# Kernel optimization log

Measured on AMD Instinct MI355X. Metric: run time of the kernel, lower is better.

Reference implementation:

```python
import jax, jax.numpy as jnp
import numpy as np

NUM_HEADS = 8
MODEL_DIM = 512
HIDDEN_DIM = 64  # model_dim // num_heads
BATCH = 4
SEQ = 1024


def setup_inputs() -> dict:
    key = jax.random.key(0)
    kx, kq, kk, kv, ko = jax.random.split(key, 5)
    # xavier_uniform bound for [model_dim, hidden_dim] fan pair
    bqkv = float(np.sqrt(6.0 / (MODEL_DIM + HIDDEN_DIM)))
    bo = float(np.sqrt(6.0 / (MODEL_DIM + MODEL_DIM)))
    return {
        "X": jax.random.normal(kx, (BATCH, SEQ, MODEL_DIM), dtype=jnp.float32),
        "mask": jnp.zeros((SEQ, SEQ), dtype=bool),  # unused by module
        "Wq": jax.random.uniform(kq, (NUM_HEADS, MODEL_DIM, HIDDEN_DIM), minval=-bqkv, maxval=bqkv, dtype=jnp.float32),
        "Wk": jax.random.uniform(kk, (NUM_HEADS, MODEL_DIM, HIDDEN_DIM), minval=-bqkv, maxval=bqkv, dtype=jnp.float32),
        "Wv": jax.random.uniform(kv, (NUM_HEADS, MODEL_DIM, HIDDEN_DIM), minval=-bqkv, maxval=bqkv, dtype=jnp.float32),
        "Wo": jax.random.uniform(ko, (MODEL_DIM, MODEL_DIM), minval=-bo, maxval=bo, dtype=jnp.float32),
    }


def reference(X, mask, Wq, Wk, Wv, Wo):
    # Per-head projections (replaces the replicated-tensor lin_proj with one einsum)
    q = jnp.einsum("bsm,hmd->hbsd", X, Wq)  # [h,b,s,d]
    k = jnp.einsum("bsm,hmd->hbsd", X, Wk)
    v = jnp.einsum("bsm,hmd->hbsd", X, Wv)
    # Katharopoulos feature map on q and k
    q = jax.nn.elu(q) + 1.0
    k = jax.nn.elu(k) + 1.0
    # Cumulative outer-product state S_t = sum_{i<=t} k_i v_i^T  -> [h,b,s,d,d]
    S = jnp.cumsum(k[..., :, None] * v[..., None, :], axis=2)
    V_bar = jnp.einsum("hbsd,hbsde->hbse", q, S)  # numerator
    Z = jnp.einsum("hbsd,hbsd->hbs", q, jnp.cumsum(k, axis=2))  # normalizer
    out_heads = V_bar / Z[..., None]  # [h,b,s,d]
    # combine_heads: permute to [b,s,h,d], flatten heads, project by Wo
    b, s = out_heads.shape[1], out_heads.shape[2]
    combined = jnp.transpose(out_heads, (1, 2, 0, 3)).reshape(b, s, -1)
    return jnp.einsum("bsm,mn->bsn", combined, Wo)
```

## Files before the change

### kernel.cpp

```cpp
#include <hip/hip_runtime.h>
#include <math.h>

namespace {
typedef unsigned short u16;
typedef __attribute__((ext_vector_type(8))) short bf16x8;
typedef __attribute__((ext_vector_type(4))) float f32x4;

constexpr int H  = 8;
constexpr int B  = 4;
constexpr int S  = 1024;
constexpr int M  = 512;
constexpr int D  = 64;
constexpr int BS = B * S;
constexpr int NC = 16;
constexpr int CH = 64;
constexpr int QSZ = H * B * S * D;
constexpr int NQKV = 3 * M;

__device__ __forceinline__ float elu1(float x) {
  return x > 0.f ? x + 1.f : __expf(x);
}

__device__ __forceinline__ u16 f2bf(float f) {
  unsigned u = __builtin_bit_cast(unsigned, f);
  u += 0x7fffu + ((u >> 16) & 1u);
  return (u16)(u >> 16);
}

__device__ __forceinline__ float bf2f(u16 v) {
  return __builtin_bit_cast(float, ((unsigned)v) << 16);
}

__device__ __forceinline__ void gload16(const u16* g, u16* l) {
  __builtin_amdgcn_global_load_lds(
      (const __attribute__((address_space(1))) unsigned int*)g,
      (__attribute__((address_space(3))) unsigned int*)l, 16, 0, 0);
}

__global__ __launch_bounds__(256) void convert_x(const float* __restrict__ X,
                                                 u16* __restrict__ Xb) {
  const int i = blockIdx.x * 256 + threadIdx.x;
  const float4 v = reinterpret_cast<const float4*>(X)[i];
  u16 o[4] = {f2bf(v.x), f2bf(v.y), f2bf(v.z), f2bf(v.w)};
  *reinterpret_cast<uint2*>(Xb + i * 4) = *reinterpret_cast<uint2*>(o);
}

__global__ __launch_bounds__(256) void build_wqkv(
    const float* __restrict__ Wq, const float* __restrict__ Wk,
    const float* __restrict__ Wv, u16* __restrict__ WCT) {
  __shared__ float t[64][65];
  const int p = blockIdx.y >> 3, h = blockIdx.y & 7;
  const float* W = ((p == 0) ? Wq : (p == 1) ? Wk : Wv) + h * (M * D);
  const int m0 = blockIdx.x * 64;
#pragma unroll
  for (int j = 0; j < 4; ++j) {
    const int i = j * 256 + threadIdx.x;
    const int mm = i >> 4, dd = (i & 15) * 4;
    const float4 v = *reinterpret_cast<const float4*>(W + (m0 + mm) * D + dd);
    t[mm][dd + 0] = v.x; t[mm][dd + 1] = v.y;
    t[mm][dd + 2] = v.z; t[mm][dd + 3] = v.w;
  }
  __syncthreads();
  const int dd = threadIdx.x >> 2, qr = (threadIdx.x & 3) * 16;
  u16* o = WCT + (p * M + h * D + dd) * M + m0 + qr;
#pragma unroll
  for (int i = 0; i < 16; ++i) o[i] = f2bf(t[qr + i][dd]);
}

__global__ __launch_bounds__(256) void build_wo(const float* __restrict__ Wo,
                                                u16* __restrict__ WoT) {
  __shared__ float t[64][65];
  const int m0 = blockIdx.x * 64, n0 = blockIdx.y * 64;
#pragma unroll
  for (int j = 0; j < 4; ++j) {
    const int i = j * 256 + threadIdx.x;
    const int mm = i >> 4, nn = (i & 15) * 4;
    const float4 v = *reinterpret_cast<const float4*>(Wo + (m0 + mm) * M + n0 + nn);
    t[mm][nn + 0] = v.x; t[mm][nn + 1] = v.y;
    t[mm][nn + 2] = v.z; t[mm][nn + 3] = v.w;
  }
  __syncthreads();
  const int nn = threadIdx.x >> 2, qr = (threadIdx.x & 3) * 16;
  u16* o = WoT + (n0 + nn) * M + m0 + qr;
#pragma unroll
  for (int i = 0; i < 16; ++i) o[i] = f2bf(t[qr + i][nn]);
}

__global__ __launch_bounds__(256) void gemm_qkv(const u16* __restrict__ A,
                                                const u16* __restrict__ BT,
                                                u16* __restrict__ qb,
                                                u16* __restrict__ kb,
                                                u16* __restrict__ kTb,
                                                u16* __restrict__ vTb) {
  __shared__ alignas(16) u16 As[128 * 32];
  __shared__ alignas(16) u16 Bs[128 * 32];
  const int tid = threadIdx.x;
  const int wave = tid >> 6, lane = tid & 63;
  const int r0 = blockIdx.x * 128, c0 = blockIdx.y * 128;
  const int wr = (wave >> 1) * 64, wc = (wave & 1) * 64;

  f32x4 acc[4][4] = {};
  const int lrow = tid >> 2;
  const int lk = (tid & 3) * 8;
  const u16* ga0 = A + (size_t)(r0 + lrow) * 512 + lk;
  const u16* ga1 = A + (size_t)(r0 + 64 + lrow) * 512 + lk;
  const u16* gb0 = BT + (size_t)(c0 + lrow) * 512 + lk;
  const u16* gb1 = BT + (size_t)(c0 + 64 + lrow) * 512 + lk;
  u16* lA0 = &As[wave * 512];
  u16* lA1 = &As[2048 + wave * 512];
  u16* lB0 = &Bs[wave * 512];
  u16* lB1 = &Bs[2048 + wave * 512];

  for (int kt = 0; kt < 16; ++kt) {
    __syncthreads();
    const int ko = kt * 32;
    gload16(ga0 + ko, lA0);
    gload16(ga1 + ko, lA1);
    gload16(gb0 + ko, lB0);
    gload16(gb1 + ko, lB1);
    __syncthreads();
    const bf16x8* As8 = reinterpret_cast<const bf16x8*>(As);
    const bf16x8* Bs8 = reinterpret_cast<const bf16x8*>(Bs);
    bf16x8 af[4], bff[4];
#pragma unroll
    for (int mf = 0; mf < 4; ++mf)
      af[mf] = As8[(wr + mf * 16 + (lane & 15)) * 4 + (lane >> 4)];
#pragma unroll
    for (int nf = 0; nf < 4; ++nf)
      bff[nf] = Bs8[(wc + nf * 16 + (lane & 15)) * 4 + (lane >> 4)];
#pragma unroll
    for (int mf = 0; mf < 4; ++mf)
#pragma unroll
      for (int nf = 0; nf < 4; ++nf)
        acc[mf][nf] = __builtin_amdgcn_mfma_f32_16x16x32_bf16(
            af[mf], bff[nf], acc[mf][nf], 0, 0, 0);
  }

#pragma unroll
  for (int nf = 0; nf < 4; ++nf) {
    const int col = c0 + wc + nf * 16 + (lane & 15);
    const int p = col >> 9, hh = (col >> 6) & 7, dd = col & 63;
#pragma unroll
    for (int mf = 0; mf < 4; ++mf) {
      const int rowb = r0 + wr + mf * 16 + (lane >> 4) * 4;
      const int b = rowb >> 10, s = rowb & 1023;
      const int hb = hh * B + b;
      u16 ov[4];
#pragma unroll
      for (int r = 0; r < 4; ++r) {
        float v = acc[mf][nf][r];
        if (p < 2) v = elu1(v);
        ov[r] = f2bf(v);
      }
      if (p == 0) {
#pragma unroll
        for (int r = 0; r < 4; ++r)
          qb[((size_t)(hb << 10) + s + r) * 64 + dd] = ov[r];
      } else if (p == 1) {
#pragma unroll
        for (int r = 0; r < 4; ++r)
          kb[((size_t)(hb << 10) + s + r) * 64 + dd] = ov[r];
        *reinterpret_cast<uint2*>(kTb + ((size_t)(hb * 64 + dd) << 10) + s) =
            *reinterpret_cast<uint2*>(ov);
      } else {
        *reinterpret_cast<uint2*>(vTb + ((size_t)(hb * 64 + dd) << 10) + s) =
            *reinterpret_cast<uint2*>(ov);
      }
    }
  }
}

__global__ __launch_bounds__(256) void gemm_out(const u16* __restrict__ A,
                                                const u16* __restrict__ BT,
                                                float* __restrict__ out) {
  __shared__ alignas(16) u16 As[128 * 32];
  __shared__ alignas(16) u16 Bs[128 * 32];
  const int tid = threadIdx.x;
  const int wave = tid >> 6, lane = tid & 63;
  const int r0 = blockIdx.x * 128, c0 = blockIdx.y * 128;
  const int wr = (wave >> 1) * 64, wc = (wave & 1) * 64;

  f32x4 acc[4][4] = {};
  const int lrow = tid >> 2;
  const int lk = (tid & 3) * 8;
  const u16* ga0 = A + (size_t)(r0 + lrow) * 512 + lk;
  const u16* ga1 = A + (size_t)(r0 + 64 + lrow) * 512 + lk;
  const u16* gb0 = BT + (size_t)(c0 + lrow) * 512 + lk;
  const u16* gb1 = BT + (size_t)(c0 + 64 + lrow) * 512 + lk;
  u16* lA0 = &As[wave * 512];
  u16* lA1 = &As[2048 + wave * 512];
  u16* lB0 = &Bs[wave * 512];
  u16* lB1 = &Bs[2048 + wave * 512];

  for (int kt = 0; kt < 16; ++kt) {
    __syncthreads();
    const int ko = kt * 32;
    gload16(ga0 + ko, lA0);
    gload16(ga1 + ko, lA1);
    gload16(gb0 + ko, lB0);
    gload16(gb1 + ko, lB1);
    __syncthreads();
    const bf16x8* As8 = reinterpret_cast<const bf16x8*>(As);
    const bf16x8* Bs8 = reinterpret_cast<const bf16x8*>(Bs);
    bf16x8 af[4], bff[4];
#pragma unroll
    for (int mf = 0; mf < 4; ++mf)
      af[mf] = As8[(wr + mf * 16 + (lane & 15)) * 4 + (lane >> 4)];
#pragma unroll
    for (int nf = 0; nf < 4; ++nf)
      bff[nf] = Bs8[(wc + nf * 16 + (lane & 15)) * 4 + (lane >> 4)];
#pragma unroll
    for (int mf = 0; mf < 4; ++mf)
#pragma unroll
      for (int nf = 0; nf < 4; ++nf)
        acc[mf][nf] = __builtin_amdgcn_mfma_f32_16x16x32_bf16(
            af[mf], bff[nf], acc[mf][nf], 0, 0, 0);
  }
#pragma unroll
  for (int nf = 0; nf < 4; ++nf) {
    const int col = c0 + wc + nf * 16 + (lane & 15);
#pragma unroll
    for (int mf = 0; mf < 4; ++mf)
#pragma unroll
      for (int r = 0; r < 4; ++r) {
        const int row = r0 + wr + mf * 16 + (lane >> 4) * 4 + r;
        out[(size_t)row * M + col] = acc[mf][nf][r];
      }
  }
}

__global__ __launch_bounds__(256) void chunkstate_mfma(
    const u16* __restrict__ kTb, const u16* __restrict__ vTb,
    float* __restrict__ G32, float* __restrict__ Ks) {
  const int tid = threadIdx.x, wave = tid >> 6, lane = tid & 63;
  const int bx = blockIdx.x, hb = bx >> 4, cc = bx & 15, s0 = cc * CH;
  const u16* vbase = vTb + ((size_t)hb * 64) * 1024 + s0;
  const u16* kbase = kTb + ((size_t)hb * 64) * 1024 + s0;

  bf16x8 av[2];
#pragma unroll
  for (int ks = 0; ks < 2; ++ks)
    av[ks] = *reinterpret_cast<const bf16x8*>(
        vbase + (size_t)(wave * 16 + (lane & 15)) * 1024 + ks * 32 + (lane >> 4) * 8);

  f32x4 acc[4] = {};
#pragma unroll
  for (int fd = 0; fd < 4; ++fd)
#pragma unroll
    for (int ks = 0; ks < 2; ++ks) {
      bf16x8 bk = *reinterpret_cast<const bf16x8*>(
          kbase + (size_t)(fd * 16 + (lane & 15)) * 1024 + ks * 32 + (lane >> 4) * 8);
      acc[fd] = __builtin_amdgcn_mfma_f32_16x16x32_bf16(av[ks], bk, acc[fd], 0, 0, 0);
    }

  float* Gp = G32 + (size_t)bx * 4096;
#pragma unroll
  for (int fd = 0; fd < 4; ++fd)
#pragma unroll
    for (int r = 0; r < 4; ++r) {
      const int e = wave * 16 + (lane >> 4) * 4 + r;
      const int d = fd * 16 + (lane & 15);
      Gp[e * 64 + d] = acc[fd][r];
    }

  const int d = tid >> 2, tq = tid & 3;
  const u16* kp = kbase + (size_t)d * 1024 + tq * 16;
  float ks = 0.f;
#pragma unroll
  for (int j = 0; j < 16; ++j) ks += bf2f(kp[j]);
  ks += __shfl_xor(ks, 1);
  ks += __shfl_xor(ks, 2);
  if (tq == 0) Ks[bx * 64 + d] = ks;
}

__global__ __launch_bounds__(256) void prefix_kernel(
    const float* __restrict__ G32, u16* __restrict__ GTb,
    float* __restrict__ Ks) {
  const int hb = blockIdx.x, eg = blockIdx.y;
  const int tid = threadIdx.x;
  const int e = eg * 4 + (tid >> 6), d = tid & 63;
  const size_t base = ((size_t)(hb * 16) * 64 + e) * 64 + d;
  float acc = 0.f;
#pragma unroll
  for (int c = 0; c < 16; ++c) {
    const float v = G32[base + (size_t)c * 4096];
    GTb[base + (size_t)c * 4096] = f2bf(acc);
    acc += v;
  }
  if (eg == 0 && tid < 64) {
    float ka = 0.f;
#pragma unroll
    for (int c = 0; c < 16; ++c) {
      const int idx = (hb * 16 + c) * 64 + tid;
      const float v = Ks[idx];
      Ks[idx] = ka;
      ka += v;
    }
  }
}

__global__ __launch_bounds__(256) void chunkout_mfma(
    const u16* __restrict__ qb, const u16* __restrict__ kb,
    const u16* __restrict__ vTb, const u16* __restrict__ GTb,
    const float* __restrict__ Kc, u16* __restrict__ att) {
  __shared__ alignas(16) u16 Qs[4096], Kls[4096], Vs[4096], Gs[4096], Astg[4096];
  const int tid = threadIdx.x, wave = tid >> 6, lane = tid & 63;
  const int bx = blockIdx.x, hb = bx >> 4, cc = bx & 15, s0 = cc * CH;
  const int h = hb >> 2, b = hb & 3;

  {
    const u16* qg = qb + ((size_t)(hb << 10) + s0) * 64;
    const u16* kg = kb + ((size_t)(hb << 10) + s0) * 64;
    const u16* gg = GTb + (size_t)bx * 4096;
#pragma unroll
    for (int j = 0; j < 2; ++j) {
      const int off = j * 2048 + wave * 512;
      gload16(qg + off + lane * 8, Qs + off);
      gload16(kg + off + lane * 8, Kls + off);
      gload16(gg + off + lane * 8, Gs + off);
    }
    const u16* vg = vTb + ((size_t)hb * 64) * 1024 + s0;
#pragma unroll
    for (int j = 0; j < 2; ++j) {
      const int e0 = j * 32 + wave * 8;
      gload16(vg + (size_t)(e0 + (lane >> 3)) * 1024 + (lane & 7) * 8,
              Vs + e0 * 64);
    }
  }
  __syncthreads();

  const bf16x8* Qs8 = reinterpret_cast<const bf16x8*>(Qs);
  const bf16x8* Ks8 = reinterpret_cast<const bf16x8*>(Kls);
  const bf16x8* Vs8 = reinterpret_cast<const bf16x8*>(Vs);
  const bf16x8* Gs8 = reinterpret_cast<const bf16x8*>(Gs);
  const bf16x8* As8 = reinterpret_cast<const bf16x8*>(Astg);

  const int i0 = wave * 16;
  const int l15 = lane & 15, lk = lane >> 4;

  bf16x8 aq[2];
#pragma unroll
  for (int ks = 0; ks < 2; ++ks)
    aq[ks] = Qs8[(i0 + l15) * 8 + ks * 4 + lk];

  f32x4 a[4] = {};
#pragma unroll
  for (int fj = 0; fj < 4; ++fj)
#pragma unroll
    for (int ks = 0; ks < 2; ++ks) {
      bf16x8 bk = Ks8[(fj * 16 + l15) * 8 + ks * 4 + lk];
      a[fj] = __builtin_amdgcn_mfma_f32_16x16x32_bf16(aq[ks], bk, a[fj], 0, 0, 0);
    }

  const float4 kc4 = *reinterpret_cast<const float4*>(Kc + bx * 64 + l15 * 4);
  float z[4];
  const int rbase = lk * 4;
#pragma unroll
  for (int r = 0; r < 4; ++r) {
    const int il = rbase + r;
    float sum = 0.f;
#pragma unroll
    for (int fj = 0; fj < 4; ++fj) {
      const int j = fj * 16 + l15;
      if (j > i0 + il) a[fj][r] = 0.f;
      sum += a[fj][r];
    }
    const uint2 qrow = *reinterpret_cast<const uint2*>(Qs + (i0 + il) * 64 + l15 * 4);
    const u16* qr16 = reinterpret_cast<const u16*>(&qrow);
    sum += bf2f(qr16[0]) * kc4.x + bf2f(qr16[1]) * kc4.y +
           bf2f(qr16[2]) * kc4.z + bf2f(qr16[3]) * kc4.w;
    z[r] = sum;
  }
#pragma unroll
  for (int off = 1; off <= 8; off <<= 1)
#pragma unroll
    for (int r = 0; r < 4; ++r) z[r] += __shfl_xor(z[r], off);

#pragma unroll
  for (int fj = 0; fj < 4; ++fj)
#pragma unroll
    for (int r = 0; r < 4; ++r)
      Astg[(i0 + rbase + r) * 64 + fj * 16 + l15] = f2bf(a[fj][r]);
  __syncthreads();

  f32x4 o[4] = {};
#pragma unroll
  for (int fe = 0; fe < 4; ++fe) {
#pragma unroll
    for (int ks = 0; ks < 2; ++ks) {
      bf16x8 bg = Gs8[(fe * 16 + l15) * 8 + ks * 4 + lk];
      o[fe] = __builtin_amdgcn_mfma_f32_16x16x32_bf16(aq[ks], bg, o[fe], 0, 0, 0);
    }
#pragma unroll
    for (int ks = 0; ks < 2; ++ks) {
      bf16x8 aa = As8[(i0 + l15) * 8 + ks * 4 + lk];
      bf16x8 bv = Vs8[(fe * 16 + l15) * 8 + ks * 4 + lk];
      o[fe] = __builtin_amdgcn_mfma_f32_16x16x32_bf16(aa, bv, o[fe], 0, 0, 0);
    }
  }

  float rz[4];
#pragma unroll
  for (int r = 0; r < 4; ++r) rz[r] = 1.f / z[r];
#pragma unroll
  for (int fe = 0; fe < 4; ++fe)
#pragma unroll
    for (int r = 0; r < 4; ++r) {
      const int srow = s0 + i0 + rbase + r;
      att[((size_t)(b << 10) + srow) * 512 + h * 64 + fe * 16 + l15] =
          f2bf(o[fe][r] * rz[r]);
    }
}

}

extern "C" void kernel_launch(void* const* d_in, const int* in_sizes, int n_in,
                              void* d_out, int out_size, void* d_ws,
                              size_t ws_size, hipStream_t stream) {
  const float* X  = (const float*)d_in[0];
  const float* Wq = (const float*)d_in[2];
  const float* Wk = (const float*)d_in[3];
  const float* Wv = (const float*)d_in[4];
  const float* Wo = (const float*)d_in[5];
  float* out = (float*)d_out;

  u16* Xb  = (u16*)d_ws;
  u16* att = Xb;
  u16* WCT = Xb + QSZ;
  u16* WoT = WCT + NQKV * M;
  u16* qb  = WoT + M * M;
  u16* kb  = qb + QSZ;
  u16* kTb = kb + QSZ;
  u16* vTb = kTb + QSZ;
  u16* GTb = vTb + QSZ;
  float* G32 = (float*)(GTb + QSZ);
  float* Ks  = G32 + QSZ;

  convert_x<<<dim3(QSZ / 1024), 256, 0, stream>>>(X, Xb);
  build_wqkv<<<dim3(8, 24), 256, 0, stream>>>(Wq, Wk, Wv, WCT);
  build_wo<<<dim3(8, 8), 256, 0, stream>>>(Wo, WoT);
  gemm_qkv<<<dim3(BS / 128, NQKV / 128), 256, 0, stream>>>(Xb, WCT, qb, kb,
                                                           kTb, vTb);
  chunkstate_mfma<<<dim3(H * B * NC), 256, 0, stream>>>(kTb, vTb, G32, Ks);
  prefix_kernel<<<dim3(H * B, 16), 256, 0, stream>>>(G32, GTb, Ks);
  chunkout_mfma<<<dim3(H * B * NC), 256, 0, stream>>>(qb, kb, vTb, GTb, Ks,
                                                      att);
  gemm_out<<<dim3(BS / 128, M / 128), 256, 0, stream>>>(att, WoT, out);
}
```

Baseline: 60.58 us.

## Merge prep kernels, fuse chunk state with prefix scan, retile both GEMMs

Folds the three input-conversion kernels into one launch that dispatches on block index. Merges the chunk-state and prefix kernels into a single per-head-batch kernel that walks the 16 chunks in order and keeps the running state in registers, which removes the fp32 intermediate buffer and one launch. Both GEMMs move to smaller output tiles (64x128 and 64x64) with a K step of 64, giving more blocks to fill the GPU. The fused state kernel launches only 32 blocks and runs its chunks one after another, which may underuse the device.

```diff
diff --git a/kernel.cpp b/kernel.cpp
--- a/kernel.cpp
+++ b/kernel.cpp
@@ -37,53 +37,54 @@
       (__attribute__((address_space(3))) unsigned int*)l, 16, 0, 0);
 }
 
-__global__ __launch_bounds__(256) void convert_x(const float* __restrict__ X,
-                                                 u16* __restrict__ Xb) {
-  const int i = blockIdx.x * 256 + threadIdx.x;
-  const float4 v = reinterpret_cast<const float4*>(X)[i];
-  u16 o[4] = {f2bf(v.x), f2bf(v.y), f2bf(v.z), f2bf(v.w)};
-  *reinterpret_cast<uint2*>(Xb + i * 4) = *reinterpret_cast<uint2*>(o);
-}
-
-__global__ __launch_bounds__(256) void build_wqkv(
-    const float* __restrict__ Wq, const float* __restrict__ Wk,
-    const float* __restrict__ Wv, u16* __restrict__ WCT) {
+__global__ __launch_bounds__(256) void prep(
+    const float* __restrict__ X, const float* __restrict__ Wq,
+    const float* __restrict__ Wk, const float* __restrict__ Wv,
+    const float* __restrict__ Wo, u16* __restrict__ Xb,
+    u16* __restrict__ WCT, u16* __restrict__ WoT) {
   __shared__ float t[64][65];
-  const int p = blockIdx.y >> 3, h = blockIdx.y & 7;
-  const float* W = ((p == 0) ? Wq : (p == 1) ? Wk : Wv) + h * (M * D);
-  const int m0 = blockIdx.x * 64;
-#pragma unroll
-  for (int j = 0; j < 4; ++j) {
-    const int i = j * 256 + threadIdx.x;
-    const int mm = i >> 4, dd = (i & 15) * 4;
-    const float4 v = *reinterpret_cast<const float4*>(W + (m0 + mm) * D + dd);
-    t[mm][dd + 0] = v.x; t[mm][dd + 1] = v.y;
-    t[mm][dd + 2] = v.z; t[mm][dd + 3] = v.w;
-  }
-  __syncthreads();
-  const int dd = threadIdx.x >> 2, qr = (threadIdx.x & 3) * 16;
-  u16* o = WCT + (p * M + h * D + dd) * M + m0 + qr;
-#pragma unroll
-  for (int i = 0; i < 16; ++i) o[i] = f2bf(t[qr + i][dd]);
-}
-
-__global__ __launch_bounds__(256) void build_wo(const float* __restrict__ Wo,
-                                                u16* __restrict__ WoT) {
-  __shared__ float t[64][65];
-  const int m0 = blockIdx.x * 64, n0 = blockIdx.y * 64;
-#pragma unroll
-  for (int j = 0; j < 4; ++j) {
-    const int i = j * 256 + threadIdx.x;
-    const int mm = i >> 4, nn = (i & 15) * 4;
-    const float4 v = *reinterpret_cast<const float4*>(Wo + (m0 + mm) * M + n0 + nn);
-    t[mm][nn + 0] = v.x; t[mm][nn + 1] = v.y;
-    t[mm][nn + 2] = v.z; t[mm][nn + 3] = v.w;
-  }
-  __syncthreads();
-  const int nn = threadIdx.x >> 2, qr = (threadIdx.x & 3) * 16;
-  u16* o = WoT + (n0 + nn) * M + m0 + qr;
-#pragma unroll
-  for (int i = 0; i < 16; ++i) o[i] = f2bf(t[qr + i][nn]);
+  const int bid = blockIdx.x;
+  if (bid < 2048) {
+    const int i = bid * 256 + threadIdx.x;
+    const float4 v = reinterpret_cast<const float4*>(X)[i];
+    u16 o[4] = {f2bf(v.x), f2bf(v.y), f2bf(v.z), f2bf(v.w)};
+    *reinterpret_cast<uint2*>(Xb + i * 4) = *reinterpret_cast<uint2*>(o);
+  } else if (bid < 2240) {
+    const int bb = bid - 2048;
+    const int mt = bb & 7, ph = bb >> 3;
+    const int p = ph >> 3, h = ph & 7;
+    const float* W = ((p == 0) ? Wq : (p == 1) ? Wk : Wv) + h * (M * D);
+    const int m0 = mt * 64;
+#pragma unroll
+    for (int j = 0; j < 4; ++j) {
+      const int i = j * 256 + threadIdx.x;
+      const int mm = i >> 4, dd = (i & 15) * 4;
+      const float4 v = *reinterpret_cast<const float4*>(W + (m0 + mm) * D + dd);
+      t[mm][dd + 0] = v.x; t[mm][dd + 1] = v.y;
+      t[mm][dd + 2] = v.z; t[mm][dd + 3] = v.w;
+    }
+    __syncthreads();
+    const int dd = threadIdx.x >> 2, qr = (threadIdx.x & 3) * 16;
+    u16* o = WCT + (p * M + h * D + dd) * M + m0 + qr;
+#pragma unroll
+    for (int i = 0; i < 16; ++i) o[i] = f2bf(t[qr + i][dd]);
+  } else {
+    const int bb = bid - 2240;
+    const int m0 = (bb & 7) * 64, n0 = (bb >> 3) * 64;
+#pragma unroll
+    for (int j = 0; j < 4; ++j) {
+      const int i = j * 256 + threadIdx.x;
+      const int mm = i >> 4, nn = (i & 15) * 4;
+      const float4 v = *reinterpret_cast<const float4*>(Wo + (m0 + mm) * M + n0 + nn);
+      t[mm][nn + 0] = v.x; t[mm][nn + 1] = v.y;
+      t[mm][nn + 2] = v.z; t[mm][nn + 3] = v.w;
+    }
+    __syncthreads();
+    const int nn = threadIdx.x >> 2, qr = (threadIdx.x & 3) * 16;
+    u16* o = WoT + (n0 + nn) * M + m0 + qr;
+#pragma unroll
+    for (int i = 0; i < 16; ++i) o[i] = f2bf(t[qr + i][nn]);
+  }
 }
 
 __global__ __launch_bounds__(256) void gemm_qkv(const u16* __restrict__ A,
@@ -92,59 +93,60 @@
                                                 u16* __restrict__ kb,
                                                 u16* __restrict__ kTb,
                                                 u16* __restrict__ vTb) {
-  __shared__ alignas(16) u16 As[128 * 32];
-  __shared__ alignas(16) u16 Bs[128 * 32];
-  const int tid = threadIdx.x;
-  const int wave = tid >> 6, lane = tid & 63;
-  const int r0 = blockIdx.x * 128, c0 = blockIdx.y * 128;
-  const int wr = (wave >> 1) * 64, wc = (wave & 1) * 64;
-
-  f32x4 acc[4][4] = {};
-  const int lrow = tid >> 2;
-  const int lk = (tid & 3) * 8;
-  const u16* ga0 = A + (size_t)(r0 + lrow) * 512 + lk;
-  const u16* ga1 = A + (size_t)(r0 + 64 + lrow) * 512 + lk;
-  const u16* gb0 = BT + (size_t)(c0 + lrow) * 512 + lk;
-  const u16* gb1 = BT + (size_t)(c0 + 64 + lrow) * 512 + lk;
-  u16* lA0 = &As[wave * 512];
-  u16* lA1 = &As[2048 + wave * 512];
-  u16* lB0 = &Bs[wave * 512];
-  u16* lB1 = &Bs[2048 + wave * 512];
-
-  for (int kt = 0; kt < 16; ++kt) {
-    __syncthreads();
-    const int ko = kt * 32;
-    gload16(ga0 + ko, lA0);
-    gload16(ga1 + ko, lA1);
-    gload16(gb0 + ko, lB0);
-    gload16(gb1 + ko, lB1);
-    __syncthreads();
-    const bf16x8* As8 = reinterpret_cast<const bf16x8*>(As);
-    const bf16x8* Bs8 = reinterpret_cast<const bf16x8*>(Bs);
-    bf16x8 af[4], bff[4];
+  __shared__ alignas(16) u16 As[64 * 64];
+  __shared__ alignas(16) u16 Bs[128 * 64];
+  const int tid = threadIdx.x, wave = tid >> 6, lane = tid & 63;
+  const int r0 = blockIdx.x * 64, c0 = blockIdx.y * 128;
+  const int l15 = lane & 15, lk = lane >> 4;
+  const int srow = wave * 8 + (lane >> 3);
+  const int sk = (lane & 7) * 8;
+
+  f32x4 acc[4][2] = {};
+  const bf16x8* As8 = reinterpret_cast<const bf16x8*>(As);
+  const bf16x8* Bs8 = reinterpret_cast<const bf16x8*>(Bs);
+
+  for (int kt = 0; kt < 8; ++kt) {
+    const int k0 = kt * 64;
+    __syncthreads();
+#pragma unroll
+    for (int j = 0; j < 2; ++j)
+      gload16(A + (size_t)(r0 + j * 32 + srow) * 512 + k0 + sk,
+              As + j * 2048 + wave * 512);
+#pragma unroll
+    for (int j = 0; j < 4; ++j)
+      gload16(BT + (size_t)(c0 + j * 32 + srow) * 512 + k0 + sk,
+              Bs + j * 2048 + wave * 512);
+    __syncthreads();
+    bf16x8 a[4][2], b[2][2];
 #pragma unroll
     for (int mf = 0; mf < 4; ++mf)
-      af[mf] = As8[(wr + mf * 16 + (lane & 15)) * 4 + (lane >> 4)];
-#pragma unroll
-    for (int nf = 0; nf < 4; ++nf)
-      bff[nf] = Bs8[(wc + nf * 16 + (lane & 15)) * 4 + (lane >> 4)];
-#pragma unroll
-    for (int mf = 0; mf < 4; ++mf)
-#pragma unroll
-      for (int nf = 0; nf < 4; ++nf)
-        acc[mf][nf] = __builtin_amdgcn_mfma_f32_16x16x32_bf16(
-            af[mf], bff[nf], acc[mf][nf], 0, 0, 0);
-  }
-
-#pragma unroll
-  for (int nf = 0; nf < 4; ++nf) {
-    const int col = c0 + wc + nf * 16 + (lane & 15);
+#pragma unroll
+      for (int ks = 0; ks < 2; ++ks)
+        a[mf][ks] = As8[(mf * 16 + l15) * 8 + ks * 4 + lk];
+#pragma unroll
+    for (int nf = 0; nf < 2; ++nf)
+#pragma unroll
+      for (int ks = 0; ks < 2; ++ks)
+        b[nf][ks] = Bs8[(wave * 32 + nf * 16 + l15) * 8 + ks * 4 + lk];
+#pragma unroll
+    for (int ks = 0; ks < 2; ++ks)
+#pragma unroll
+      for (int mf = 0; mf < 4; ++mf)
+#pragma unroll
+        for (int nf = 0; nf < 2; ++nf)
+          acc[mf][nf] = __builtin_amdgcn_mfma_f32_16x16x32_bf16(
+              a[mf][ks], b[nf][ks], acc[mf][nf], 0, 0, 0);
+  }
+
+#pragma unroll
+  for (int nf = 0; nf < 2; ++nf) {
+    const int col = c0 + wave * 32 + nf * 16 + l15;
     const int p = col >> 9, hh = (col >> 6) & 7, dd = col & 63;
 #pragma unroll
     for (int mf = 0; mf < 4; ++mf) {
-      const int rowb = r0 + wr + mf * 16 + (lane >> 4) * 4;
-      const int b = rowb >> 10, s = rowb & 1023;
-      const int hb = hh * B + b;
+      const int rowb = r0 + mf * 16 + lk * 4;
+      const int b_ = rowb >> 10, s = rowb & 1023;
+      const int hb = hh * B + b_;
       u16 ov[4];
 #pragma unroll
       for (int r = 0; r < 4; ++r) {
@@ -173,129 +175,120 @@
 __global__ __launch_bounds__(256) void gemm_out(const u16* __restrict__ A,
                                                 const u16* __restrict__ BT,
                                                 float* __restrict__ out) {
-  __shared__ alignas(16) u16 As[128 * 32];
-  __shared__ alignas(16) u16 Bs[128 * 32];
-  const int tid = threadIdx.x;
-  const int wave = tid >> 6, lane = tid & 63;
-  const int r0 = blockIdx.x * 128, c0 = blockIdx.y * 128;
-  const int wr = (wave >> 1) * 64, wc = (wave & 1) * 64;
-
-  f32x4 acc[4][4] = {};
-  const int lrow = tid >> 2;
-  const int lk = (tid & 3) * 8;
-  const u16* ga0 = A + (size_t)(r0 + lrow) * 512 + lk;
-  const u16* ga1 = A + (size_t)(r0 + 64 + lrow) * 512 + lk;
-  const u16* gb0 = BT + (size_t)(c0 + lrow) * 512 + lk;
-  const u16* gb1 = BT + (size_t)(c0 + 64 + lrow) * 512 + lk;
-  u16* lA0 = &As[wave * 512];
-  u16* lA1 = &As[2048 + wave * 512];
-  u16* lB0 = &Bs[wave * 512];
-  u16* lB1 = &Bs[2048 + wave * 512];
-
-  for (int kt = 0; kt < 16; ++kt) {
-    __syncthreads();
-    const int ko = kt * 32;
-    gload16(ga0 + ko, lA0);
-    gload16(ga1 + ko, lA1);
-    gload16(gb0 + ko, lB0);
-    gload16(gb1 + ko, lB1);
-    __syncthreads();
-    const bf16x8* As8 = reinterpret_cast<const bf16x8*>(As);
-    const bf16x8* Bs8 = reinterpret_cast<const bf16x8*>(Bs);
-    bf16x8 af[4], bff[4];
-#pragma unroll
-    for (int mf = 0; mf < 4; ++mf)
-      af[mf] = As8[(wr + mf * 16 + (lane & 15)) * 4 + (lane >> 4)];
-#pragma unroll
-    for (int nf = 0; nf < 4; ++nf)
-      bff[nf] = Bs8[(wc + nf * 16 + (lane & 15)) * 4 + (lane >> 4)];
-#pragma unroll
-    for (int mf = 0; mf < 4; ++mf)
-#pragma unroll
-      for (int nf = 0; nf < 4; ++nf)
-        acc[mf][nf] = __builtin_amdgcn_mfma_f32_16x16x32_bf16(
-            af[mf], bff[nf], acc[mf][nf], 0, 0, 0);
-  }
-#pragma unroll
-  for (int nf = 0; nf < 4; ++nf) {
-    const int col = c0 + wc + nf * 16 + (lane & 15);
-#pragma unroll
-    for (int mf = 0; mf < 4; ++mf)
+  __shared__ alignas(16) u16 As[64 * 64];
+  __shared__ alignas(16) u16 Bs[64 * 64];
+  const int tid = threadIdx.x, wave = tid >> 6, lane = tid & 63;
+  const int r0 = blockIdx.x * 64, c0 = blockIdx.y * 64;
+  const int wr = (wave >> 1) * 32, wc = (wave & 1) * 32;
+  const int l15 = lane & 15, lk = lane >> 4;
+  const int srow = wave * 8 + (lane >> 3);
+  const int sk = (lane & 7) * 8;
+
+  f32x4 acc[2][2] = {};
+  const bf16x8* As8 = reinterpret_cast<const bf16x8*>(As);
+  const bf16x8* Bs8 = reinterpret_cast<const bf16x8*>(Bs);
+
+  for (int kt = 0; kt < 8; ++kt) {
+    const int k0 = kt * 64;
+    __syncthreads();
+#pragma unroll
+    for (int j = 0; j < 2; ++j) {
+      gload16(A + (size_t)(r0 + j * 32 + srow) * 512 + k0 + sk,
+              As + j * 2048 + wave * 512);
+      gload16(BT + (size_t)(c0 + j * 32 + srow) * 512 + k0 + sk,
+              Bs + j * 2048 + wave * 512);
+    }
+    __syncthreads();
+    bf16x8 a[2][2], b[2][2];
+#pragma unroll
+    for (int mf = 0; mf < 2; ++mf)
+#pragma unroll
+      for (int ks = 0; ks < 2; ++ks)
+        a[mf][ks] = As8[(wr + mf * 16 + l15) * 8 + ks * 4 + lk];
+#pragma unroll
+    for (int nf = 0; nf < 2; ++nf)
+#pragma unroll
+      for (int ks = 0; ks < 2; ++ks)
+        b[nf][ks] = Bs8[(wc + nf * 16 + l15) * 8 + ks * 4 + lk];
+#pragma unroll
+    for (int ks = 0; ks < 2; ++ks)
+#pragma unroll
+      for (int mf = 0; mf < 2; ++mf)
+#pragma unroll
+        for (int nf = 0; nf < 2; ++nf)
+          acc[mf][nf] = __builtin_amdgcn_mfma_f32_16x16x32_bf16(
+              a[mf][ks], b[nf][ks], acc[mf][nf], 0, 0, 0);
+  }
+#pragma unroll
+  for (int nf = 0; nf < 2; ++nf) {
+    const int col = c0 + wc + nf * 16 + l15;
+#pragma unroll
+    for (int mf = 0; mf < 2; ++mf)
 #pragma unroll
       for (int r = 0; r < 4; ++r) {
-        const int row = r0 + wr + mf * 16 + (lane >> 4) * 4 + r;
+        const int row = r0 + wr + mf * 16 + lk * 4 + r;
         out[(size_t)row * M + col] = acc[mf][nf][r];
       }
   }
 }
 
-__global__ __launch_bounds__(256) void chunkstate_mfma(
+__global__ __launch_bounds__(256) void stateprefix(
     const u16* __restrict__ kTb, const u16* __restrict__ vTb,
-    float* __restrict__ G32, float* __restrict__ Ks) {
+    u16* __restrict__ GTb, float* __restrict__ Ks) {
   const int tid = threadIdx.x, wave = tid >> 6, lane = tid & 63;
-  const int bx = blockIdx.x, hb = bx >> 4, cc = bx & 15, s0 = cc * CH;
-  const u16* vbase = vTb + ((size_t)hb * 64) * 1024 + s0;
-  const u16* kbase = kTb + ((size_t)hb * 64) * 1024 + s0;
-
-  bf16x8 av[2];
-#pragma unroll
-  for (int ks = 0; ks < 2; ++ks)
-    av[ks] = *reinterpret_cast<const bf16x8*>(
-        vbase + (size_t)(wave * 16 + (lane & 15)) * 1024 + ks * 32 + (lane >> 4) * 8);
-
-  f32x4 acc[4] = {};
-#pragma unroll
-  for (int fd = 0; fd < 4; ++fd)
-#pragma unroll
-    for (int ks = 0; ks < 2; ++ks) {
-      bf16x8 bk = *reinterpret_cast<const bf16x8*>(
-          kbase + (size_t)(fd * 16 + (lane & 15)) * 1024 + ks * 32 + (lane >> 4) * 8);
-      acc[fd] = __builtin_amdgcn_mfma_f32_16x16x32_bf16(av[ks], bk, acc[fd], 0, 0, 0);
-    }
-
-  float* Gp = G32 + (size_t)bx * 4096;
-#pragma unroll
-  for (int fd = 0; fd < 4; ++fd)
-#pragma unroll
-    for (int r = 0; r < 4; ++r) {
-      const int e = wave * 16 + (lane >> 4) * 4 + r;
-      const int d = fd * 16 + (lane & 15);
-      Gp[e * 64 + d] = acc[fd][r];
-    }
-
-  const int d = tid >> 2, tq = tid & 3;
-  const u16* kp = kbase + (size_t)d * 1024 + tq * 16;
-  float ks = 0.f;
-#pragma unroll
-  for (int j = 0; j < 16; ++j) ks += bf2f(kp[j]);
-  ks += __shfl_xor(ks, 1);
-  ks += __shfl_xor(ks, 2);
-  if (tq == 0) Ks[bx * 64 + d] = ks;
-}
-
-__global__ __launch_bounds__(256) void prefix_kernel(
-    const float* __restrict__ G32, u16* __restrict__ GTb,
-    float* __restrict__ Ks) {
-  const int hb = blockIdx.x, eg = blockIdx.y;
-  const int tid = threadIdx.x;
-  const int e = eg * 4 + (tid >> 6), d = tid & 63;
-  const size_t base = ((size_t)(hb * 16) * 64 + e) * 64 + d;
-  float acc = 0.f;
-#pragma unroll
-  for (int c = 0; c < 16; ++c) {
-    const float v = G32[base + (size_t)c * 4096];
-    GTb[base + (size_t)c * 4096] = f2bf(acc);
-    acc += v;
-  }
-  if (eg == 0 && tid < 64) {
-    float ka = 0.f;
-#pragma unroll
-    for (int c = 0; c < 16; ++c) {
-      const int idx = (hb * 16 + c) * 64 + tid;
-      const float v = Ks[idx];
-      Ks[idx] = ka;
-      ka += v;
-    }
+  const int hb = blockIdx.x;
+  const int l15 = lane & 15, lk = lane >> 4;
+  const u16* vbase = vTb + ((size_t)hb * 64) * 1024;
+  const u16* kbase = kTb + ((size_t)hb * 64) * 1024;
+
+  f32x4 P[4] = {};
+  float kcum[4] = {0.f, 0.f, 0.f, 0.f};
+
+  for (int cc = 0; cc < 16; ++cc) {
+    const int s0 = cc * 64;
+    bf16x8 av[2];
+#pragma unroll
+    for (int ks = 0; ks < 2; ++ks)
+      av[ks] = *reinterpret_cast<const bf16x8*>(
+          vbase + (size_t)(wave * 16 + l15) * 1024 + s0 + ks * 32 + lk * 8);
+
+    f32x4 acc[4] = {};
+    float kp[4];
+#pragma unroll
+    for (int fd = 0; fd < 4; ++fd) {
+      float sum = 0.f;
+#pragma unroll
+      for (int ks = 0; ks < 2; ++ks) {
+        bf16x8 bk = *reinterpret_cast<const bf16x8*>(
+            kbase + (size_t)(fd * 16 + l15) * 1024 + s0 + ks * 32 + lk * 8);
+        acc[fd] = __builtin_amdgcn_mfma_f32_16x16x32_bf16(av[ks], bk, acc[fd],
+                                                          0, 0, 0);
+#pragma unroll
+        for (int e = 0; e < 8; ++e) sum += bf2f((u16)bk[e]);
+      }
+      kp[fd] = sum;
+    }
+#pragma unroll
+    for (int fd = 0; fd < 4; ++fd) {
+      kp[fd] += __shfl_xor(kp[fd], 16);
+      kp[fd] += __shfl_xor(kp[fd], 32);
+    }
+    u16* gp = GTb + (size_t)(hb * 16 + cc) * 4096;
+#pragma unroll
+    for (int fd = 0; fd < 4; ++fd)
+#pragma unroll
+      for (int r = 0; r < 4; ++r)
+        gp[(wave * 16 + lk * 4 + r) * 64 + fd * 16 + l15] = f2bf(P[fd][r]);
+#pragma unroll
+    for (int fd = 0; fd < 4; ++fd) P[fd] += acc[fd];
+
+    if (wave == 0 && lk == 0) {
+#pragma unroll
+      for (int fd = 0; fd < 4; ++fd)
+        Ks[(hb * 16 + cc) * 64 + fd * 16 + l15] = kcum[fd];
+    }
+#pragma unroll
+    for (int fd = 0; fd < 4; ++fd) kcum[fd] += kp[fd];
   }
 }
 
@@ -433,17 +426,13 @@
   u16* kTb = kb + QSZ;
   u16* vTb = kTb + QSZ;
   u16* GTb = vTb + QSZ;
-  float* G32 = (float*)(GTb + QSZ);
-  float* Ks  = G32 + QSZ;
-
-  convert_x<<<dim3(QSZ / 1024), 256, 0, stream>>>(X, Xb);
-  build_wqkv<<<dim3(8, 24), 256, 0, stream>>>(Wq, Wk, Wv, WCT);
-  build_wo<<<dim3(8, 8), 256, 0, stream>>>(Wo, WoT);
-  gemm_qkv<<<dim3(BS / 128, NQKV / 128), 256, 0, stream>>>(Xb, WCT, qb, kb,
-                                                           kTb, vTb);
-  chunkstate_mfma<<<dim3(H * B * NC), 256, 0, stream>>>(kTb, vTb, G32, Ks);
-  prefix_kernel<<<dim3(H * B, 16), 256, 0, stream>>>(G32, GTb, Ks);
+  float* Ks = (float*)(GTb + QSZ);
+
+  prep<<<dim3(2304), 256, 0, stream>>>(X, Wq, Wk, Wv, Wo, Xb, WCT, WoT);
+  gemm_qkv<<<dim3(BS / 64, NQKV / 128), 256, 0, stream>>>(Xb, WCT, qb, kb,
+                                                          kTb, vTb);
+  stateprefix<<<dim3(H * B), 256, 0, stream>>>(kTb, vTb, GTb, Ks);
   chunkout_mfma<<<dim3(H * B * NC), 256, 0, stream>>>(qb, kb, vTb, GTb, Ks,
                                                       att);
-  gemm_out<<<dim3(BS / 128, M / 128), 256, 0, stream>>>(att, WoT, out);
-}
+  gemm_out<<<dim3(BS / 64, M / 64), 256, 0, stream>>>(att, WoT, out);
+}
```

Result: slower. 67.51 us (+11.4%).

## Fuse prep kernels, double-buffer GEMM LDS tiles, shrink output GEMM tile

Applied to the files above, without the earlier changes.

Merges the X conversion and the two weight transpose/convert kernels into one `prep` launch that dispatches on block index. Both bf16 GEMMs now double-buffer their LDS tiles, so the next k-slice is loaded while the current one runs on MFMA, with one barrier per iteration instead of two. The output GEMM uses a 128x64 tile, doubling its block count for better CU occupancy. A barrier between the Astg store and the MFMA stage in `chunkout_mfma` is also dropped. That is only safe if each wave reads back only the rows it wrote itself, so it risks a data race.

```diff
diff --git a/kernel.cpp b/kernel.cpp
--- a/kernel.cpp
+++ b/kernel.cpp
@@ -37,53 +37,54 @@
       (__attribute__((address_space(3))) unsigned int*)l, 16, 0, 0);
 }
 
-__global__ __launch_bounds__(256) void convert_x(const float* __restrict__ X,
-                                                 u16* __restrict__ Xb) {
-  const int i = blockIdx.x * 256 + threadIdx.x;
-  const float4 v = reinterpret_cast<const float4*>(X)[i];
-  u16 o[4] = {f2bf(v.x), f2bf(v.y), f2bf(v.z), f2bf(v.w)};
-  *reinterpret_cast<uint2*>(Xb + i * 4) = *reinterpret_cast<uint2*>(o);
-}
-
-__global__ __launch_bounds__(256) void build_wqkv(
-    const float* __restrict__ Wq, const float* __restrict__ Wk,
-    const float* __restrict__ Wv, u16* __restrict__ WCT) {
+__global__ __launch_bounds__(256) void prep(
+    const float* __restrict__ X, const float* __restrict__ Wq,
+    const float* __restrict__ Wk, const float* __restrict__ Wv,
+    const float* __restrict__ Wo, u16* __restrict__ Xb,
+    u16* __restrict__ WCT, u16* __restrict__ WoT) {
   __shared__ float t[64][65];
-  const int p = blockIdx.y >> 3, h = blockIdx.y & 7;
-  const float* W = ((p == 0) ? Wq : (p == 1) ? Wk : Wv) + h * (M * D);
-  const int m0 = blockIdx.x * 64;
-#pragma unroll
-  for (int j = 0; j < 4; ++j) {
-    const int i = j * 256 + threadIdx.x;
-    const int mm = i >> 4, dd = (i & 15) * 4;
-    const float4 v = *reinterpret_cast<const float4*>(W + (m0 + mm) * D + dd);
-    t[mm][dd + 0] = v.x; t[mm][dd + 1] = v.y;
-    t[mm][dd + 2] = v.z; t[mm][dd + 3] = v.w;
-  }
-  __syncthreads();
-  const int dd = threadIdx.x >> 2, qr = (threadIdx.x & 3) * 16;
-  u16* o = WCT + (p * M + h * D + dd) * M + m0 + qr;
-#pragma unroll
-  for (int i = 0; i < 16; ++i) o[i] = f2bf(t[qr + i][dd]);
-}
-
-__global__ __launch_bounds__(256) void build_wo(const float* __restrict__ Wo,
-                                                u16* __restrict__ WoT) {
-  __shared__ float t[64][65];
-  const int m0 = blockIdx.x * 64, n0 = blockIdx.y * 64;
-#pragma unroll
-  for (int j = 0; j < 4; ++j) {
-    const int i = j * 256 + threadIdx.x;
-    const int mm = i >> 4, nn = (i & 15) * 4;
-    const float4 v = *reinterpret_cast<const float4*>(Wo + (m0 + mm) * M + n0 + nn);
-    t[mm][nn + 0] = v.x; t[mm][nn + 1] = v.y;
-    t[mm][nn + 2] = v.z; t[mm][nn + 3] = v.w;
-  }
-  __syncthreads();
-  const int nn = threadIdx.x >> 2, qr = (threadIdx.x & 3) * 16;
-  u16* o = WoT + (n0 + nn) * M + m0 + qr;
-#pragma unroll
-  for (int i = 0; i < 16; ++i) o[i] = f2bf(t[qr + i][nn]);
+  const int bid = blockIdx.x;
+  if (bid < 2048) {
+    const int i = bid * 256 + threadIdx.x;
+    const float4 v = reinterpret_cast<const float4*>(X)[i];
+    u16 o[4] = {f2bf(v.x), f2bf(v.y), f2bf(v.z), f2bf(v.w)};
+    *reinterpret_cast<uint2*>(Xb + i * 4) = *reinterpret_cast<uint2*>(o);
+  } else if (bid < 2240) {
+    const int bb = bid - 2048;
+    const int mt = bb & 7, ph = bb >> 3;
+    const int p = ph >> 3, h = ph & 7;
+    const float* W = ((p == 0) ? Wq : (p == 1) ? Wk : Wv) + h * (M * D);
+    const int m0 = mt * 64;
+#pragma unroll
+    for (int j = 0; j < 4; ++j) {
+      const int i = j * 256 + threadIdx.x;
+      const int mm = i >> 4, dd = (i & 15) * 4;
+      const float4 v = *reinterpret_cast<const float4*>(W + (m0 + mm) * D + dd);
+      t[mm][dd + 0] = v.x; t[mm][dd + 1] = v.y;
+      t[mm][dd + 2] = v.z; t[mm][dd + 3] = v.w;
+    }
+    __syncthreads();
+    const int dd = threadIdx.x >> 2, qr = (threadIdx.x & 3) * 16;
+    u16* o = WCT + (p * M + h * D + dd) * M + m0 + qr;
+#pragma unroll
+    for (int i = 0; i < 16; ++i) o[i] = f2bf(t[qr + i][dd]);
+  } else {
+    const int bb = bid - 2240;
+    const int m0 = (bb & 7) * 64, n0 = (bb >> 3) * 64;
+#pragma unroll
+    for (int j = 0; j < 4; ++j) {
+      const int i = j * 256 + threadIdx.x;
+      const int mm = i >> 4, nn = (i & 15) * 4;
+      const float4 v = *reinterpret_cast<const float4*>(Wo + (m0 + mm) * M + n0 + nn);
+      t[mm][nn + 0] = v.x; t[mm][nn + 1] = v.y;
+      t[mm][nn + 2] = v.z; t[mm][nn + 3] = v.w;
+    }
+    __syncthreads();
+    const int nn = threadIdx.x >> 2, qr = (threadIdx.x & 3) * 16;
+    u16* o = WoT + (n0 + nn) * M + m0 + qr;
+#pragma unroll
+    for (int i = 0; i < 16; ++i) o[i] = f2bf(t[qr + i][nn]);
+  }
 }
 
 __global__ __launch_bounds__(256) void gemm_qkv(const u16* __restrict__ A,
@@ -92,8 +93,8 @@
                                                 u16* __restrict__ kb,
                                                 u16* __restrict__ kTb,
                                                 u16* __restrict__ vTb) {
-  __shared__ alignas(16) u16 As[128 * 32];
-  __shared__ alignas(16) u16 Bs[128 * 32];
+  __shared__ alignas(16) u16 As[2][4096];
+  __shared__ alignas(16) u16 Bs[2][4096];
   const int tid = threadIdx.x;
   const int wave = tid >> 6, lane = tid & 63;
   const int r0 = blockIdx.x * 128, c0 = blockIdx.y * 128;
@@ -106,21 +107,22 @@
   const u16* ga1 = A + (size_t)(r0 + 64 + lrow) * 512 + lk;
   const u16* gb0 = BT + (size_t)(c0 + lrow) * 512 + lk;
   const u16* gb1 = BT + (size_t)(c0 + 64 + lrow) * 512 + lk;
-  u16* lA0 = &As[wave * 512];
-  u16* lA1 = &As[2048 + wave * 512];
-  u16* lB0 = &Bs[wave * 512];
-  u16* lB1 = &Bs[2048 + wave * 512];
-
+
+#define STG_QKV(kt, b)                                \
+  {                                                   \
+    const int ko = (kt) * 32;                         \
+    gload16(ga0 + ko, &As[b][wave * 512]);            \
+    gload16(ga1 + ko, &As[b][2048 + wave * 512]);     \
+    gload16(gb0 + ko, &Bs[b][wave * 512]);            \
+    gload16(gb1 + ko, &Bs[b][2048 + wave * 512]);     \
+  }
+
+  STG_QKV(0, 0);
+  __syncthreads();
   for (int kt = 0; kt < 16; ++kt) {
-    __syncthreads();
-    const int ko = kt * 32;
-    gload16(ga0 + ko, lA0);
-    gload16(ga1 + ko, lA1);
-    gload16(gb0 + ko, lB0);
-    gload16(gb1 + ko, lB1);
-    __syncthreads();
-    const bf16x8* As8 = reinterpret_cast<const bf16x8*>(As);
-    const bf16x8* Bs8 = reinterpret_cast<const bf16x8*>(Bs);
+    if (kt < 15) STG_QKV(kt + 1, (kt + 1) & 1);
+    const bf16x8* As8 = reinterpret_cast<const bf16x8*>(As[kt & 1]);
+    const bf16x8* Bs8 = reinterpret_cast<const bf16x8*>(Bs[kt & 1]);
     bf16x8 af[4], bff[4];
 #pragma unroll
     for (int mf = 0; mf < 4; ++mf)
@@ -134,7 +136,9 @@
       for (int nf = 0; nf < 4; ++nf)
         acc[mf][nf] = __builtin_amdgcn_mfma_f32_16x16x32_bf16(
             af[mf], bff[nf], acc[mf][nf], 0, 0, 0);
-  }
+    __syncthreads();
+  }
+#undef STG_QKV
 
 #pragma unroll
   for (int nf = 0; nf < 4; ++nf) {
@@ -173,51 +177,53 @@
 __global__ __launch_bounds__(256) void gemm_out(const u16* __restrict__ A,
                                                 const u16* __restrict__ BT,
                                                 float* __restrict__ out) {
-  __shared__ alignas(16) u16 As[128 * 32];
-  __shared__ alignas(16) u16 Bs[128 * 32];
+  __shared__ alignas(16) u16 As[2][4096];
+  __shared__ alignas(16) u16 Bs[2][2048];
   const int tid = threadIdx.x;
   const int wave = tid >> 6, lane = tid & 63;
-  const int r0 = blockIdx.x * 128, c0 = blockIdx.y * 128;
-  const int wr = (wave >> 1) * 64, wc = (wave & 1) * 64;
-
-  f32x4 acc[4][4] = {};
+  const int r0 = blockIdx.x * 128, c0 = blockIdx.y * 64;
+  const int wr = (wave >> 1) * 64, wc = (wave & 1) * 32;
+
+  f32x4 acc[4][2] = {};
   const int lrow = tid >> 2;
   const int lk = (tid & 3) * 8;
   const u16* ga0 = A + (size_t)(r0 + lrow) * 512 + lk;
   const u16* ga1 = A + (size_t)(r0 + 64 + lrow) * 512 + lk;
   const u16* gb0 = BT + (size_t)(c0 + lrow) * 512 + lk;
-  const u16* gb1 = BT + (size_t)(c0 + 64 + lrow) * 512 + lk;
-  u16* lA0 = &As[wave * 512];
-  u16* lA1 = &As[2048 + wave * 512];
-  u16* lB0 = &Bs[wave * 512];
-  u16* lB1 = &Bs[2048 + wave * 512];
-
+
+#define STG_OUT(kt, b)                                \
+  {                                                   \
+    const int ko = (kt) * 32;                         \
+    gload16(ga0 + ko, &As[b][wave * 512]);            \
+    gload16(ga1 + ko, &As[b][2048 + wave * 512]);     \
+    if (wave < 4) gload16(gb0 + ko, &Bs[b][wave * 512]); \
+  }
+
+  STG_OUT(0, 0);
+  __syncthreads();
   for (int kt = 0; kt < 16; ++kt) {
+    if (kt < 15) STG_OUT(kt + 1, (kt + 1) & 1);
+    const bf16x8* As8 = reinterpret_cast<const bf16x8*>(As[kt & 1]);
+    const bf16x8* Bs8 = reinterpret_cast<const bf16x8*>(Bs[kt & 1]);
+    bf16x8 a[4], b[2];
+#pragma unroll
+    for (int mf = 0; mf < 4; ++mf)
+      a[mf] = As8[(wr + mf * 16 + (lane & 15)) * 4 + (lane >> 4)];
+#pragma unroll
+    for (int nf = 0; nf < 2; ++nf)
+      b[nf] = Bs8[(wc + nf * 16 + (lane & 15)) * 4 + (lane >> 4)];
+#pragma unroll
+    for (int mf = 0; mf < 4; ++mf)
+#pragma unroll
+      for (int nf = 0; nf < 2; ++nf)
+        acc[mf][nf] = __builtin_amdgcn_mfma_f32_16x16x32_bf16(
+            a[mf], b[nf], acc[mf][nf], 0, 0, 0);
     __syncthreads();
-    const int ko = kt * 32;
-    gload16(ga0 + ko, lA0);
-    gload16(ga1 + ko, lA1);
-    gload16(gb0 + ko, lB0);
-    gload16(gb1 + ko, lB1);
-    __syncthreads();
-    const bf16x8* As8 = reinterpret_cast<const bf16x8*>(As);
-    const bf16x8* Bs8 = reinterpret_cast<const bf16x8*>(Bs);
-    bf16x8 af[4], bff[4];
-#pragma unroll
-    for (int mf = 0; mf < 4; ++mf)
-      af[mf] = As8[(wr + mf * 16 + (lane & 15)) * 4 + (lane >> 4)];
-#pragma unroll
-    for (int nf = 0; nf < 4; ++nf)
-      bff[nf] = Bs8[(wc + nf * 16 + (lane & 15)) * 4 + (lane >> 4)];
-#pragma unroll
-    for (int mf = 0; mf < 4; ++mf)
-#pragma unroll
-      for (int nf = 0; nf < 4; ++nf)
-        acc[mf][nf] = __builtin_amdgcn_mfma_f32_16x16x32_bf16(
-            af[mf], bff[nf], acc[mf][nf], 0, 0, 0);
-  }
-#pragma unroll
-  for (int nf = 0; nf < 4; ++nf) {
+  }
+#undef STG_OUT
+
+#pragma unroll
+  for (int nf = 0; nf < 2; ++nf) {
     const int col = c0 + wc + nf * 16 + (lane & 15);
 #pragma unroll
     for (int mf = 0; mf < 4; ++mf)
@@ -381,7 +387,6 @@
 #pragma unroll
     for (int r = 0; r < 4; ++r)
       Astg[(i0 + rbase + r) * 64 + fj * 16 + l15] = f2bf(a[fj][r]);
-  __syncthreads();
 
   f32x4 o[4] = {};
 #pragma unroll
@@ -436,14 +441,12 @@
   float* G32 = (float*)(GTb + QSZ);
   float* Ks  = G32 + QSZ;
 
-  convert_x<<<dim3(QSZ / 1024), 256, 0, stream>>>(X, Xb);
-  build_wqkv<<<dim3(8, 24), 256, 0, stream>>>(Wq, Wk, Wv, WCT);
-  build_wo<<<dim3(8, 8), 256, 0, stream>>>(Wo, WoT);
+  prep<<<dim3(2304), 256, 0, stream>>>(X, Wq, Wk, Wv, Wo, Xb, WCT, WoT);
   gemm_qkv<<<dim3(BS / 128, NQKV / 128), 256, 0, stream>>>(Xb, WCT, qb, kb,
                                                            kTb, vTb);
   chunkstate_mfma<<<dim3(H * B * NC), 256, 0, stream>>>(kTb, vTb, G32, Ks);
   prefix_kernel<<<dim3(H * B, 16), 256, 0, stream>>>(G32, GTb, Ks);
   chunkout_mfma<<<dim3(H * B * NC), 256, 0, stream>>>(qb, kb, vTb, GTb, Ks,
                                                       att);
-  gemm_out<<<dim3(BS / 128, M / 128), 256, 0, stream>>>(att, WoT, out);
-}
+  gemm_out<<<dim3(BS / 128, M / 64), 256, 0, stream>>>(att, WoT, out);
+}
```

Result: faster. 52.63 us (-13.1%).
